# Optimization experiments

Measured on AMD Instinct MI355X. Metric: run time of the kernel, lower is better.

Reference implementation:

```python
import jax, jax.numpy as jnp
import numpy as np

N_NODES = 100000
N_EDGES = 1600000
D_IN = 128
D_HID = 128


def gcn_conv(x, src, dst, W, b, n_nodes):
    """PyG-style GCNConv: out = D^{-1/2} (A + I) D^{-1/2} (x @ W) + b.

    src/dst already include self-loops.
    """
    deg = jax.ops.segment_sum(jnp.ones_like(src, dtype=x.dtype), dst,
                              num_segments=n_nodes)
    dinv = jnp.where(deg > 0, deg ** -0.5, 0.0)
    norm = dinv[src] * dinv[dst]              # [E]
    h = x @ W                                  # [N, d_out]
    msg = h[src] * norm[:, None]               # gather + scale, [E, d_out]
    out = jax.ops.segment_sum(msg, dst, num_segments=n_nodes)
    return out + b


def setup_inputs() -> dict:
    key = jax.random.key(0)
    k1, k2, k3, k4 = jax.random.split(key, 4)
    x = jax.random.normal(k1, (N_NODES, D_IN), dtype=jnp.float32)
    edge_index = jax.random.randint(k2, (2, N_EDGES), 0, N_NODES, dtype=jnp.int64)
    s1 = (1.0 / np.sqrt(D_IN)).astype(np.float32)
    s2 = (1.0 / np.sqrt(D_HID)).astype(np.float32)
    W1 = jax.random.normal(k3, (D_IN, D_HID), dtype=jnp.float32) * s1
    b1 = jnp.zeros((D_HID,), dtype=jnp.float32)
    W2 = jax.random.normal(k4, (D_HID, D_HID), dtype=jnp.float32) * s2
    b2 = jnp.zeros((D_HID,), dtype=jnp.float32)
    return {"x": x, "edge_index": edge_index, "W1": W1, "b1": b1,
            "W2": W2, "b2": b2}


def reference(x, edge_index, W1, b1, W2, b2):
    n_nodes = x.shape[0]
    loops = jnp.arange(n_nodes, dtype=edge_index.dtype)
    src = jnp.concatenate([edge_index[0], loops])  # self-loops, as PyG default
    dst = jnp.concatenate([edge_index[1], loops])
    h = gcn_conv(x, src, dst, W1, b1, n_nodes)
    h = gcn_conv(h, src, dst, W2, b2, n_nodes)
    return h
```

## Files before the change

kernel.cpp:

```cpp
#include <hip/hip_runtime.h>

#define N_NODES 100000
#define N_EDGES 1600000

#define NBIN 196
#define BINCAP 9216
#define NPB 4096
#define PBLK ((N_EDGES + NPB - 1) / NPB)

typedef unsigned int uint;
typedef unsigned short u16;
typedef __attribute__((ext_vector_type(8))) short bf16x8;
typedef __attribute__((ext_vector_type(4))) float f32x4;

__device__ __forceinline__ uint bf16_rtne(float f) {
  uint u = __float_as_uint(f);
  return (u + 0x7fffu + ((u >> 16) & 1u)) >> 16;
}


__global__ __launch_bounds__(256) void k_zerobc(int* __restrict__ bin_cur) {
  if (threadIdx.x < NBIN) bin_cur[threadIdx.x] = 0;
}

__global__ __launch_bounds__(256) void k_part(const int* __restrict__ ei, int* __restrict__ bin_cur,
                                              uint* __restrict__ stage) {
  __shared__ uint hist[NBIN];
  __shared__ uint lcur[NBIN];
  __shared__ uint base[NBIN];
  const int t = threadIdx.x;
  const int e0 = blockIdx.x * NPB;
  for (int i = t; i < NBIN; i += 256) { hist[i] = 0; lcur[i] = 0; }
  __syncthreads();
#pragma unroll
  for (int j = 0; j < NPB / 256; ++j) {
    int e = e0 + j * 256 + t;
    if (e < N_EDGES) atomicAdd(&hist[((uint)ei[N_EDGES + e]) >> 9], 1u);
  }
  __syncthreads();
  for (int i = t; i < NBIN; i += 256)
    base[i] = hist[i] ? atomicAdd((uint*)&bin_cur[i], hist[i]) : 0u;
  __syncthreads();
#pragma unroll
  for (int j = 0; j < NPB / 256; ++j) {
    int e = e0 + j * 256 + t;
    if (e < N_EDGES) {
      uint s = (uint)ei[e];
      uint d = (uint)ei[N_EDGES + e];
      uint b = d >> 9;
      uint l = atomicAdd(&lcur[b], 1u);
      uint pos = base[b] + l;
      if (pos < BINCAP)
        stage[(size_t)b * BINCAP + pos] = s | ((d & 511u) << 17);
    }
  }
}

__global__ __launch_bounds__(256) void k_binscan(const int* __restrict__ bin_cur,
                                                 int* __restrict__ ebase, int* __restrict__ rowptr) {
  __shared__ int sd[256];
  const int t = threadIdx.x;
  int v = (t < NBIN) ? min(bin_cur[t], BINCAP) : 0;
  int s = v;
  sd[t] = s;
  __syncthreads();
  for (int off = 1; off < 256; off <<= 1) {
    int a = (t >= off) ? sd[t - off] : 0;
    __syncthreads();
    sd[t] += a;
    __syncthreads();
  }
  if (t < NBIN) ebase[t] = sd[t] - v;
  if (t == 255) rowptr[N_NODES] = sd[255];
}

__global__ __launch_bounds__(256) void k_bin2a(const int* __restrict__ bin_cur, const uint* __restrict__ stage,
                                               const int* __restrict__ ebase,
                                               float* __restrict__ dinv, int* __restrict__ rowptr) {
  __shared__ int cnt[512];
  __shared__ int sd[256];
  const int b = blockIdx.x, t = threadIdx.x;
  cnt[t] = 0; cnt[t + 256] = 0;
  __syncthreads();
  const int n = min(bin_cur[b], BINCAP);
  const uint* sb = stage + (size_t)b * BINCAP;
  for (int i = t; i < n; i += 256) atomicAdd(&cnt[sb[i] >> 17], 1);
  __syncthreads();
  int v0 = cnt[t * 2], v1 = cnt[t * 2 + 1];
  int s = v0 + v1;
  sd[t] = s;
  __syncthreads();
  for (int off = 1; off < 256; off <<= 1) {
    int a = (t >= off) ? sd[t - off] : 0;
    __syncthreads();
    sd[t] += a;
    __syncthreads();
  }
  int run = sd[t] - s;
  int g0 = b * 512 + t * 2;
  int eb = ebase[b];
  if (g0 < N_NODES) {
    rowptr[g0] = eb + run;
    dinv[g0] = rsqrtf((float)(v0 + 1));
  }
  if (g0 + 1 < N_NODES) {
    rowptr[g0 + 1] = eb + run + v0;
    dinv[g0 + 1] = rsqrtf((float)(v1 + 1));
  }
}

__global__ __launch_bounds__(256) void k_bin2b(const int* __restrict__ bin_cur, const uint* __restrict__ stage,
                                               const int* __restrict__ rowptr, const float* __restrict__ dinv,
                                               int2* __restrict__ ep) {
  __shared__ int cur[512];
  const int b = blockIdx.x, t = threadIdx.x;
  const int g0 = b * 512;
  for (int l = t; l < 512; l += 256) {
    int g = g0 + l;
    cur[l] = (g < N_NODES) ? rowptr[g] : 0;
  }
  __syncthreads();
  const int n = min(bin_cur[b], BINCAP);
  const uint* sb = stage + (size_t)b * BINCAP;
  for (int i = t; i < n; i += 256) {
    uint u = sb[i];
    int s = (int)(u & 0x1FFFFu);
    int l = (int)(u >> 17);
    float w = dinv[s];
    int pos = atomicAdd(&cur[l], 1);
    int2 pr;
    pr.x = s;
    pr.y = __float_as_int(w);
    ep[pos] = pr;
  }
}


__global__ __launch_bounds__(256) void k_prepw(const float* __restrict__ W1, const float* __restrict__ W2,
                                               uint* __restrict__ S1, uint* __restrict__ S2) {
  int u = blockIdx.x * 256 + threadIdx.x;
  const float* W = blockIdx.y ? W2 : W1;
  uint* S = blockIdx.y ? S2 : S1;
  int lane = u & 63;
  int kcnt = u >> 6;
  int kc = kcnt & 3;
  int nt = kcnt >> 2;
  int n = nt * 16 + (lane & 15);
  int k0 = kc * 32 + (lane >> 4) * 8;
  float f[8];
#pragma unroll
  for (int j = 0; j < 8; ++j) f[j] = W[(size_t)(k0 + j) * 128 + n];
  uint4 pk;
  pk.x = bf16_rtne(f[0]) | (bf16_rtne(f[1]) << 16);
  pk.y = bf16_rtne(f[2]) | (bf16_rtne(f[3]) << 16);
  pk.z = bf16_rtne(f[4]) | (bf16_rtne(f[5]) << 16);
  pk.w = bf16_rtne(f[6]) | (bf16_rtne(f[7]) << 16);
  ((uint4*)S)[u] = pk;
}


__global__ __launch_bounds__(256) void k_gemm(const void* __restrict__ Ain, int a_f32,
                                              const uint* __restrict__ Wsw,
                                              u16* __restrict__ OutH, int nrows) {
  __shared__ uint As[4096];
  __shared__ uint Bs[8192];
  const int tid = threadIdx.x;
  const int R = blockIdx.x * 64;
  {
    const uint4* src = (const uint4*)Wsw;
    uint4* dst = (uint4*)Bs;
#pragma unroll
    for (int v = 0; v < 8; ++v) dst[tid + v * 256] = src[tid + v * 256];
  }
  const int unit = tid & 15;
  const int kc_s = unit >> 2;
  const int quad_s = unit & 3;
#pragma unroll
  for (int pass = 0; pass < 4; ++pass) {
    int row = pass * 16 + (tid >> 4);
    int gr = R + row;
    if (gr >= nrows) gr = nrows - 1;
    uint4 pk;
    if (a_f32) {
      const float* srcr = (const float*)Ain + (size_t)gr * 128 + unit * 8;
      float4 f0 = ((const float4*)srcr)[0];
      float4 f1 = ((const float4*)srcr)[1];
      pk.x = bf16_rtne(f0.x) | (bf16_rtne(f0.y) << 16);
      pk.y = bf16_rtne(f0.z) | (bf16_rtne(f0.w) << 16);
      pk.z = bf16_rtne(f1.x) | (bf16_rtne(f1.y) << 16);
      pk.w = bf16_rtne(f1.z) | (bf16_rtne(f1.w) << 16);
    } else {
      pk = ((const uint4*)((const uint*)Ain + (size_t)gr * 64))[unit];
    }
    int lane_t = quad_s * 16 + (row & 15);
    *(uint4*)&As[((pass * 4 + kc_s) * 64 + lane_t) * 4] = pk;
  }
  __syncthreads();

  const int w = tid >> 6;
  const int lane = tid & 63;
  bf16x8 a0 = *(bf16x8*)&As[((w * 4 + 0) * 64 + lane) * 4];
  bf16x8 a1 = *(bf16x8*)&As[((w * 4 + 1) * 64 + lane) * 4];
  bf16x8 a2 = *(bf16x8*)&As[((w * 4 + 2) * 64 + lane) * 4];
  bf16x8 a3 = *(bf16x8*)&As[((w * 4 + 3) * 64 + lane) * 4];
  f32x4 acc[8];
#pragma unroll
  for (int nt = 0; nt < 8; ++nt) acc[nt] = (f32x4){0.f, 0.f, 0.f, 0.f};
#pragma unroll
  for (int nt = 0; nt < 8; ++nt) {
    bf16x8 b0 = *(bf16x8*)&Bs[((nt * 4 + 0) * 64 + lane) * 4];
    bf16x8 b1 = *(bf16x8*)&Bs[((nt * 4 + 1) * 64 + lane) * 4];
    bf16x8 b2 = *(bf16x8*)&Bs[((nt * 4 + 2) * 64 + lane) * 4];
    bf16x8 b3 = *(bf16x8*)&Bs[((nt * 4 + 3) * 64 + lane) * 4];
    acc[nt] = __builtin_amdgcn_mfma_f32_16x16x32_bf16(a0, b0, acc[nt], 0, 0, 0);
    acc[nt] = __builtin_amdgcn_mfma_f32_16x16x32_bf16(a1, b1, acc[nt], 0, 0, 0);
    acc[nt] = __builtin_amdgcn_mfma_f32_16x16x32_bf16(a2, b2, acc[nt], 0, 0, 0);
    acc[nt] = __builtin_amdgcn_mfma_f32_16x16x32_bf16(a3, b3, acc[nt], 0, 0, 0);
  }
  const int colb = lane & 15;
  const int quad = lane >> 4;
#pragma unroll
  for (int nt = 0; nt < 8; ++nt) {
#pragma unroll
    for (int r = 0; r < 4; ++r) {
      int gr = R + w * 16 + quad * 4 + r;
      if (gr < nrows)
        OutH[(size_t)gr * 128 + nt * 16 + colb] = (u16)bf16_rtne(acc[nt][r]);
    }
  }
}


__device__ __forceinline__ void bacc(float& ax, float& ay, uint v, float w) {
  ax += w * __uint_as_float(v << 16);
  ay += w * __uint_as_float(v & 0xffff0000u);
}

__global__ __launch_bounds__(256) void k_agg(const uint* __restrict__ hb, const float* __restrict__ dinv,
                                             const int* __restrict__ rowptr, const int2* __restrict__ ep,
                                             const float* __restrict__ bias,
                                             u16* __restrict__ outb, float* __restrict__ outf) {
  int wid = threadIdx.x >> 6;
  int lane = threadIdx.x & 63;
  int node = blockIdx.x * 4 + wid;
  if (node >= N_NODES) return;
  int beg = rowptr[node];
  int end = rowptr[node + 1];
  float dn = dinv[node];
  uint selfv = hb[(size_t)node * 64 + lane];
  float ax = 0.f, ay = 0.f;
  bacc(ax, ay, selfv, dn);

  int e = beg;
  for (; e + 8 <= end; e += 8) {
    int2 p[8];
#pragma unroll
    for (int j = 0; j < 8; ++j) p[j] = ep[e + j];
    uint v[8];
#pragma unroll
    for (int j = 0; j < 8; ++j) v[j] = hb[(size_t)p[j].x * 64 + lane];
#pragma unroll
    for (int j = 0; j < 8; ++j) bacc(ax, ay, v[j], __int_as_float(p[j].y));
  }
  if (e + 4 <= end) {
    int2 p[4];
#pragma unroll
    for (int j = 0; j < 4; ++j) p[j] = ep[e + j];
    uint v[4];
#pragma unroll
    for (int j = 0; j < 4; ++j) v[j] = hb[(size_t)p[j].x * 64 + lane];
#pragma unroll
    for (int j = 0; j < 4; ++j) bacc(ax, ay, v[j], __int_as_float(p[j].y));
    e += 4;
  }
  for (; e < end; ++e) {
    int2 p = ep[e];
    uint v = hb[(size_t)p.x * 64 + lane];
    bacc(ax, ay, v, __int_as_float(p.y));
  }

  int c = lane * 2;
  float rx = dn * ax + bias[c];
  float ry = dn * ay + bias[c + 1];
  if (outb) {
    uint pk = bf16_rtne(rx) | (bf16_rtne(ry) << 16);
    *(uint*)(outb + (size_t)node * 128 + c) = pk;
  } else {
    float2 o; o.x = rx; o.y = ry;
    *(float2*)(outf + (size_t)node * 128 + c) = o;
  }
}


extern "C" void kernel_launch(void* const* d_in, const int* in_sizes, int n_in,
                              void* d_out, int out_size, void* d_ws, size_t ws_size,
                              hipStream_t stream) {
  const float* x  = (const float*)d_in[0];
  const int*   ei = (const int*)d_in[1];
  const float* W1 = (const float*)d_in[2];
  const float* b1 = (const float*)d_in[3];
  const float* W2 = (const float*)d_in[4];
  const float* b2 = (const float*)d_in[5];
  float* out = (float*)d_out;

  char* p = (char*)d_ws;
  uint*  hb     = (uint*)p;  p += (size_t)N_NODES * 64 * sizeof(uint);
  int2*  ep     = (int2*)p;  p += (size_t)N_EDGES * sizeof(int2);
  uint*  stage  = (uint*)p;  p += (size_t)NBIN * BINCAP * sizeof(uint);
  uint*  wsw1   = (uint*)p;  p += 8192 * sizeof(uint);
  uint*  wsw2   = (uint*)p;  p += 8192 * sizeof(uint);
  float* dinv   = (float*)p; p += (size_t)N_NODES * sizeof(float);
  int*   rowptr = (int*)p;   p += (size_t)(N_NODES + 1) * sizeof(int);
  int*   bin_cur= (int*)p;   p += (size_t)NBIN * sizeof(int);
  int*   ebase  = (int*)p;   p += (size_t)NBIN * sizeof(int);

  u16* h1b = (u16*)d_out;

  const int GG = (N_NODES + 63) / 64;

  k_zerobc<<<1, 256, 0, stream>>>(bin_cur);
  k_part<<<PBLK, 256, 0, stream>>>(ei, bin_cur, stage);
  k_binscan<<<1, 256, 0, stream>>>(bin_cur, ebase, rowptr);
  k_bin2a<<<NBIN, 256, 0, stream>>>(bin_cur, stage, ebase, dinv, rowptr);
  k_bin2b<<<NBIN, 256, 0, stream>>>(bin_cur, stage, rowptr, dinv, ep);
  k_prepw<<<dim3(8, 2), 256, 0, stream>>>(W1, W2, wsw1, wsw2);

  k_gemm<<<GG, 256, 0, stream>>>(x, 1, wsw1, (u16*)hb, N_NODES);
  k_agg<<<(N_NODES + 3) / 4, 256, 0, stream>>>(hb, dinv, rowptr, ep, b1, h1b, nullptr);
  k_gemm<<<GG, 256, 0, stream>>>(h1b, 0, wsw2, (u16*)hb, N_NODES);
  k_agg<<<(N_NODES + 3) / 4, 256, 0, stream>>>(hb, dinv, rowptr, ep, b2, nullptr, out);
}
```

Before: 334.6 us.

## Fuse layer-1 aggregation with layer-2 GEMM and merge CSR build kernels

Adds k_aggm, which aggregates 16 nodes per block into LDS as bf16 and then applies the second weight matrix with MFMA. This removes the separate second GEMM and its round trip of the intermediate through global memory. The CSR build now merges the two bin kernels into one that keeps staged entries in registers. Edge records shrink to the source index only, so dinv[src] is gathered during aggregation. k_part also gets per-wave histograms to cut shared atomic contention. The trade-off is an extra dinv gather per edge, and stage/hb2 now share the same workspace region.

```diff
diff --git a/kernel.cpp b/kernel.cpp
--- a/kernel.cpp
+++ b/kernel.cpp
@@ -6,6 +6,8 @@
 #define NBIN 196
 #define BINCAP 9216
 #define NPB 4096
+#define EPT 16
+#define BPT 36
 #define PBLK ((N_EDGES + NPB - 1) / NPB)
 
 typedef unsigned int uint;
@@ -25,33 +27,41 @@
 
 __global__ __launch_bounds__(256) void k_part(const int* __restrict__ ei, int* __restrict__ bin_cur,
                                               uint* __restrict__ stage) {
-  __shared__ uint hist[NBIN];
-  __shared__ uint lcur[NBIN];
-  __shared__ uint base[NBIN];
+  __shared__ uint hist[4][NBIN];
+  __shared__ uint wbase[4][NBIN];
+  __shared__ uint lcur[4][NBIN];
   const int t = threadIdx.x;
+  const int w = t >> 6;
   const int e0 = blockIdx.x * NPB;
-  for (int i = t; i < NBIN; i += 256) { hist[i] = 0; lcur[i] = 0; }
-  __syncthreads();
-#pragma unroll
-  for (int j = 0; j < NPB / 256; ++j) {
+  for (int i = t; i < 4 * NBIN; i += 256) { (&hist[0][0])[i] = 0; (&lcur[0][0])[i] = 0; }
+  __syncthreads();
+  uint d[EPT];
+#pragma unroll
+  for (int j = 0; j < EPT; ++j) {
     int e = e0 + j * 256 + t;
-    if (e < N_EDGES) atomicAdd(&hist[((uint)ei[N_EDGES + e]) >> 9], 1u);
-  }
-  __syncthreads();
-  for (int i = t; i < NBIN; i += 256)
-    base[i] = hist[i] ? atomicAdd((uint*)&bin_cur[i], hist[i]) : 0u;
-  __syncthreads();
-#pragma unroll
-  for (int j = 0; j < NPB / 256; ++j) {
-    int e = e0 + j * 256 + t;
-    if (e < N_EDGES) {
+    d[j] = (e < N_EDGES) ? (uint)ei[N_EDGES + e] : 0xFFFFFFFFu;
+    if (d[j] != 0xFFFFFFFFu) atomicAdd(&hist[w][d[j] >> 9], 1u);
+  }
+  __syncthreads();
+  if (t < NBIN) {
+    uint h0 = hist[0][t], h1 = hist[1][t], h2 = hist[2][t], h3 = hist[3][t];
+    uint tot = h0 + h1 + h2 + h3;
+    uint g = tot ? (uint)atomicAdd(&bin_cur[t], (int)tot) : 0u;
+    wbase[0][t] = g;
+    wbase[1][t] = g + h0;
+    wbase[2][t] = g + h0 + h1;
+    wbase[3][t] = g + h0 + h1 + h2;
+  }
+  __syncthreads();
+#pragma unroll
+  for (int j = 0; j < EPT; ++j) {
+    if (d[j] != 0xFFFFFFFFu) {
+      int e = e0 + j * 256 + t;
       uint s = (uint)ei[e];
-      uint d = (uint)ei[N_EDGES + e];
-      uint b = d >> 9;
-      uint l = atomicAdd(&lcur[b], 1u);
-      uint pos = base[b] + l;
+      uint b = d[j] >> 9;
+      uint pos = wbase[w][b] + atomicAdd(&lcur[w][b], 1u);
       if (pos < BINCAP)
-        stage[(size_t)b * BINCAP + pos] = s | ((d & 511u) << 17);
+        stage[(size_t)b * BINCAP + pos] = s | ((d[j] & 511u) << 17);
     }
   }
 }
@@ -74,17 +84,27 @@
   if (t == 255) rowptr[N_NODES] = sd[255];
 }
 
-__global__ __launch_bounds__(256) void k_bin2a(const int* __restrict__ bin_cur, const uint* __restrict__ stage,
-                                               const int* __restrict__ ebase,
-                                               float* __restrict__ dinv, int* __restrict__ rowptr) {
+__global__ __launch_bounds__(256) void k_bin2(const int* __restrict__ bin_cur, const uint* __restrict__ stage,
+                                              const int* __restrict__ ebase,
+                                              float* __restrict__ dinv, int* __restrict__ rowptr,
+                                              int* __restrict__ ep) {
   __shared__ int cnt[512];
   __shared__ int sd[256];
+  __shared__ int curs[512];
   const int b = blockIdx.x, t = threadIdx.x;
   cnt[t] = 0; cnt[t + 256] = 0;
   __syncthreads();
   const int n = min(bin_cur[b], BINCAP);
   const uint* sb = stage + (size_t)b * BINCAP;
-  for (int i = t; i < n; i += 256) atomicAdd(&cnt[sb[i] >> 17], 1);
+  uint r[BPT];
+#pragma unroll
+  for (int j = 0; j < BPT; ++j) {
+    int i = j * 256 + t;
+    r[j] = (i < n) ? sb[i] : 0xFFFFFFFFu;
+  }
+#pragma unroll
+  for (int j = 0; j < BPT; ++j)
+    if (r[j] != 0xFFFFFFFFu) atomicAdd(&cnt[r[j] >> 17], 1);
   __syncthreads();
   int v0 = cnt[t * 2], v1 = cnt[t * 2 + 1];
   int s = v0 + v1;
@@ -97,42 +117,25 @@
     __syncthreads();
   }
   int run = sd[t] - s;
+  int eb = ebase[b];
+  int c0 = eb + run, c1 = eb + run + v0;
   int g0 = b * 512 + t * 2;
-  int eb = ebase[b];
   if (g0 < N_NODES) {
-    rowptr[g0] = eb + run;
+    rowptr[g0] = c0;
     dinv[g0] = rsqrtf((float)(v0 + 1));
   }
   if (g0 + 1 < N_NODES) {
-    rowptr[g0 + 1] = eb + run + v0;
+    rowptr[g0 + 1] = c1;
     dinv[g0 + 1] = rsqrtf((float)(v1 + 1));
   }
-}
-
-__global__ __launch_bounds__(256) void k_bin2b(const int* __restrict__ bin_cur, const uint* __restrict__ stage,
-                                               const int* __restrict__ rowptr, const float* __restrict__ dinv,
-                                               int2* __restrict__ ep) {
-  __shared__ int cur[512];
-  const int b = blockIdx.x, t = threadIdx.x;
-  const int g0 = b * 512;
-  for (int l = t; l < 512; l += 256) {
-    int g = g0 + l;
-    cur[l] = (g < N_NODES) ? rowptr[g] : 0;
-  }
-  __syncthreads();
-  const int n = min(bin_cur[b], BINCAP);
-  const uint* sb = stage + (size_t)b * BINCAP;
-  for (int i = t; i < n; i += 256) {
-    uint u = sb[i];
-    int s = (int)(u & 0x1FFFFu);
-    int l = (int)(u >> 17);
-    float w = dinv[s];
-    int pos = atomicAdd(&cur[l], 1);
-    int2 pr;
-    pr.x = s;
-    pr.y = __float_as_int(w);
-    ep[pos] = pr;
-  }
+  curs[t * 2] = c0; curs[t * 2 + 1] = c1;
+  __syncthreads();
+#pragma unroll
+  for (int j = 0; j < BPT; ++j)
+    if (r[j] != 0xFFFFFFFFu) {
+      int pos = atomicAdd(&curs[r[j] >> 17], 1);
+      ep[pos] = (int)(r[j] & 0x1FFFFu);
+    }
 }
 
 
@@ -236,10 +239,104 @@
   ay += w * __uint_as_float(v & 0xffff0000u);
 }
 
+__device__ __forceinline__ void agg_node(const uint* __restrict__ hb, const float* __restrict__ dinv,
+                                         const int* __restrict__ ep, int node, int lane,
+                                         int beg, int end, float dn, float& ax, float& ay) {
+  uint selfv = hb[(size_t)node * 64 + lane];
+  bacc(ax, ay, selfv, dn);
+  int e = beg;
+  for (; e + 8 <= end; e += 8) {
+    int p[8];
+#pragma unroll
+    for (int j = 0; j < 8; ++j) p[j] = ep[e + j];
+    float wt[8];
+#pragma unroll
+    for (int j = 0; j < 8; ++j) wt[j] = dinv[p[j]];
+    uint v[8];
+#pragma unroll
+    for (int j = 0; j < 8; ++j) v[j] = hb[(size_t)p[j] * 64 + lane];
+#pragma unroll
+    for (int j = 0; j < 8; ++j) bacc(ax, ay, v[j], wt[j]);
+  }
+  if (e + 4 <= end) {
+    int p[4];
+#pragma unroll
+    for (int j = 0; j < 4; ++j) p[j] = ep[e + j];
+    float wt[4];
+#pragma unroll
+    for (int j = 0; j < 4; ++j) wt[j] = dinv[p[j]];
+    uint v[4];
+#pragma unroll
+    for (int j = 0; j < 4; ++j) v[j] = hb[(size_t)p[j] * 64 + lane];
+#pragma unroll
+    for (int j = 0; j < 4; ++j) bacc(ax, ay, v[j], wt[j]);
+    e += 4;
+  }
+  for (; e < end; ++e) {
+    int p = ep[e];
+    float wt = dinv[p];
+    uint v = hb[(size_t)p * 64 + lane];
+    bacc(ax, ay, v, wt);
+  }
+}
+
+
+__global__ __launch_bounds__(256) void k_aggm(const uint* __restrict__ hb, const float* __restrict__ dinv,
+                                              const int* __restrict__ rowptr, const int* __restrict__ ep,
+                                              const float* __restrict__ bias, const uint* __restrict__ Wsw,
+                                              u16* __restrict__ outH) {
+  __shared__ uint Abf[16 * 64];
+  const int w = threadIdx.x >> 6;
+  const int lane = threadIdx.x & 63;
+  const int nb = blockIdx.x * 16;
+#pragma unroll 1
+  for (int j = 0; j < 4; ++j) {
+    const int lr = w * 4 + j;
+    const int node = nb + lr;
+    const int beg = rowptr[node];
+    const int end = rowptr[node + 1];
+    const float dn = dinv[node];
+    float ax = 0.f, ay = 0.f;
+    agg_node(hb, dinv, ep, node, lane, beg, end, dn, ax, ay);
+    int c = lane * 2;
+    float rx = dn * ax + bias[c];
+    float ry = dn * ay + bias[c + 1];
+    uint pk = bf16_rtne(rx) | (bf16_rtne(ry) << 16);
+    Abf[(lr * 64 + lane) ^ ((lr & 7) << 2)] = pk;
+  }
+  __syncthreads();
+  const int row = lane & 15;
+  const int kq = lane >> 4;
+  bf16x8 a[4];
+#pragma unroll
+  for (int kc = 0; kc < 4; ++kc) {
+    int ui = row * 64 + kc * 16 + kq * 4;
+    a[kc] = *(bf16x8*)&Abf[ui ^ ((row & 7) << 2)];
+  }
+  const int colb = lane & 15;
+  const int quad = lane >> 4;
+#pragma unroll
+  for (int nt2 = 0; nt2 < 2; ++nt2) {
+    const int nt = w * 2 + nt2;
+    f32x4 acc = (f32x4){0.f, 0.f, 0.f, 0.f};
+#pragma unroll
+    for (int kc = 0; kc < 4; ++kc) {
+      bf16x8 bfr = *(const bf16x8*)((const uint4*)Wsw + (nt * 4 + kc) * 64 + lane);
+      acc = __builtin_amdgcn_mfma_f32_16x16x32_bf16(a[kc], bfr, acc, 0, 0, 0);
+    }
+#pragma unroll
+    for (int r2 = 0; r2 < 4; ++r2) {
+      int gr = nb + quad * 4 + r2;
+      outH[(size_t)gr * 128 + nt * 16 + colb] = (u16)bf16_rtne(acc[r2]);
+    }
+  }
+}
+
+
 __global__ __launch_bounds__(256) void k_agg(const uint* __restrict__ hb, const float* __restrict__ dinv,
-                                             const int* __restrict__ rowptr, const int2* __restrict__ ep,
+                                             const int* __restrict__ rowptr, const int* __restrict__ ep,
                                              const float* __restrict__ bias,
-                                             u16* __restrict__ outb, float* __restrict__ outf) {
+                                             float* __restrict__ outf) {
   int wid = threadIdx.x >> 6;
   int lane = threadIdx.x & 63;
   int node = blockIdx.x * 4 + wid;
@@ -247,48 +344,13 @@
   int beg = rowptr[node];
   int end = rowptr[node + 1];
   float dn = dinv[node];
-  uint selfv = hb[(size_t)node * 64 + lane];
   float ax = 0.f, ay = 0.f;
-  bacc(ax, ay, selfv, dn);
-
-  int e = beg;
-  for (; e + 8 <= end; e += 8) {
-    int2 p[8];
-#pragma unroll
-    for (int j = 0; j < 8; ++j) p[j] = ep[e + j];
-    uint v[8];
-#pragma unroll
-    for (int j = 0; j < 8; ++j) v[j] = hb[(size_t)p[j].x * 64 + lane];
-#pragma unroll
-    for (int j = 0; j < 8; ++j) bacc(ax, ay, v[j], __int_as_float(p[j].y));
-  }
-  if (e + 4 <= end) {
-    int2 p[4];
-#pragma unroll
-    for (int j = 0; j < 4; ++j) p[j] = ep[e + j];
-    uint v[4];
-#pragma unroll
-    for (int j = 0; j < 4; ++j) v[j] = hb[(size_t)p[j].x * 64 + lane];
-#pragma unroll
-    for (int j = 0; j < 4; ++j) bacc(ax, ay, v[j], __int_as_float(p[j].y));
-    e += 4;
-  }
-  for (; e < end; ++e) {
-    int2 p = ep[e];
-    uint v = hb[(size_t)p.x * 64 + lane];
-    bacc(ax, ay, v, __int_as_float(p.y));
-  }
-
+  agg_node(hb, dinv, ep, node, lane, beg, end, dn, ax, ay);
   int c = lane * 2;
-  float rx = dn * ax + bias[c];
-  float ry = dn * ay + bias[c + 1];
-  if (outb) {
-    uint pk = bf16_rtne(rx) | (bf16_rtne(ry) << 16);
-    *(uint*)(outb + (size_t)node * 128 + c) = pk;
-  } else {
-    float2 o; o.x = rx; o.y = ry;
-    *(float2*)(outf + (size_t)node * 128 + c) = o;
-  }
+  float2 o;
+  o.x = dn * ax + bias[c];
+  o.y = dn * ay + bias[c + 1];
+  *(float2*)(outf + (size_t)node * 128 + c) = o;
 }
 
 
@@ -305,28 +367,26 @@
 
   char* p = (char*)d_ws;
   uint*  hb     = (uint*)p;  p += (size_t)N_NODES * 64 * sizeof(uint);
-  int2*  ep     = (int2*)p;  p += (size_t)N_EDGES * sizeof(int2);
-  uint*  stage  = (uint*)p;  p += (size_t)NBIN * BINCAP * sizeof(uint);
+  int*   ep     = (int*)p;   p += (size_t)N_EDGES * sizeof(int);
   uint*  wsw1   = (uint*)p;  p += 8192 * sizeof(uint);
   uint*  wsw2   = (uint*)p;  p += 8192 * sizeof(uint);
   float* dinv   = (float*)p; p += (size_t)N_NODES * sizeof(float);
   int*   rowptr = (int*)p;   p += (size_t)(N_NODES + 1) * sizeof(int);
   int*   bin_cur= (int*)p;   p += (size_t)NBIN * sizeof(int);
   int*   ebase  = (int*)p;   p += (size_t)NBIN * sizeof(int);
-
-  u16* h1b = (u16*)d_out;
+  p = (char*)(((uintptr_t)p + 63) & ~(uintptr_t)63);
+  uint*  stage  = (uint*)p;
+  uint*  hb2    = (uint*)p;
 
   const int GG = (N_NODES + 63) / 64;
 
   k_zerobc<<<1, 256, 0, stream>>>(bin_cur);
   k_part<<<PBLK, 256, 0, stream>>>(ei, bin_cur, stage);
   k_binscan<<<1, 256, 0, stream>>>(bin_cur, ebase, rowptr);
-  k_bin2a<<<NBIN, 256, 0, stream>>>(bin_cur, stage, ebase, dinv, rowptr);
-  k_bin2b<<<NBIN, 256, 0, stream>>>(bin_cur, stage, rowptr, dinv, ep);
+  k_bin2<<<NBIN, 256, 0, stream>>>(bin_cur, stage, ebase, dinv, rowptr, ep);
   k_prepw<<<dim3(8, 2), 256, 0, stream>>>(W1, W2, wsw1, wsw2);
 
   k_gemm<<<GG, 256, 0, stream>>>(x, 1, wsw1, (u16*)hb, N_NODES);
-  k_agg<<<(N_NODES + 3) / 4, 256, 0, stream>>>(hb, dinv, rowptr, ep, b1, h1b, nullptr);
-  k_gemm<<<GG, 256, 0, stream>>>(h1b, 0, wsw2, (u16*)hb, N_NODES);
-  k_agg<<<(N_NODES + 3) / 4, 256, 0, stream>>>(hb, dinv, rowptr, ep, b2, nullptr, out);
-}
+  k_aggm<<<N_NODES / 16, 256, 0, stream>>>(hb, dinv, rowptr, ep, b1, wsw2, (u16*)hb2);
+  k_agg<<<(N_NODES + 3) / 4, 256, 0, stream>>>(hb2, dinv, rowptr, ep, b2, out);
+}
```

Result: faster. 319.0 us (-4.7%).
